# Kernel tuning notes

Measured on AMD Instinct MI355X. Metric: run time of the kernel, lower is better.

Reference implementation:

```python
import jax, jax.numpy as jnp
import numpy as np

NUM_CLASSES = 10
WEIGHT = tuple([0.1] * NUM_CLASSES)
EXPONENT = 2


def setup_inputs() -> dict:
    key = jax.random.key(0)
    k1, k2, k3 = jax.random.split(key, 3)
    B, Y, X = 64, 512, 512
    outputs = jax.random.normal(k1, (B, Y, X), dtype=jnp.float32)
    # targets hold integer intensity classes 0..9 stored as floats (original does float subtraction)
    targets = jax.random.randint(k2, (B, Y, X), 0, NUM_CLASSES).astype(jnp.float32)
    # observation-station mask: 1 where a station exists, 0 elsewhere
    mask = jax.random.randint(k3, (B, Y, X), 0, 2).astype(jnp.int32)
    return {"outputs": outputs, "targets": targets, "mask": mask}


def reference(outputs, targets, mask):
    # Class id per pixel; invalid (mask==0) pixels routed to dummy segment NUM_CLASSES.
    cls = targets.astype(jnp.int32)
    valid = mask == 1
    ids = jnp.where(valid, cls, NUM_CLASSES).ravel()  # [B*Y*X]

    sqerr = (outputs - targets) ** EXPONENT  # [B,Y,X]
    # One fused scatter-reduce replaces the original triple Python loop over 10 masks.
    per_class_sum = jax.ops.segment_sum(sqerr.ravel(), ids, num_segments=NUM_CLASSES + 1)[:NUM_CLASSES]
    class_n = jax.ops.segment_sum(jnp.ones_like(sqerr).ravel(), ids, num_segments=NUM_CLASSES + 1)[:NUM_CLASSES]

    loss_each = jnp.where(class_n > 0, per_class_sum / jnp.maximum(class_n, 1.0), 0.0)  # [10]
    weight = jnp.asarray(WEIGHT, dtype=outputs.dtype)
    loss = jnp.sum(weight * loss_each)
    return loss, loss_each, class_n
```

## Files before the change

kernel.cpp:

```cpp
#include <hip/hip_runtime.h>

#define NCLS 10
#define TPB  256
#define NBLK 2048
#define ACC_STRIDE 64

typedef float vfloat4 __attribute__((ext_vector_type(4)));
typedef int   vint4   __attribute__((ext_vector_type(4)));


__device__ __forceinline__ void proc_elem(float o, float t, int m,
                                          float sum[NCLS], unsigned long long &cnt)
{
    float d  = o - t;
    float sq = d * d;
    int cls  = (m == 1) ? (int)t : NCLS;
    cnt += 1ull << (6 * cls);
#pragma unroll
    for (int c = 0; c < NCLS; ++c)
        sum[c] += (cls == c) ? sq : 0.0f;
}

__global__ __launch_bounds__(TPB) void loss_main_kernel(
    const float* __restrict__ outputs,
    const float* __restrict__ targets,
    const int*   __restrict__ mask,
    float* __restrict__ ws,
    int n4, int n_rem_base, int n_rem)
{
    const vfloat4* o4 = (const vfloat4*)outputs;
    const vfloat4* t4 = (const vfloat4*)targets;
    const vint4*   m4 = (const vint4*)mask;

    const int tid = blockIdx.x * TPB + threadIdx.x;
    const int T   = NBLK * TPB;

    float sum[NCLS];
#pragma unroll
    for (int c = 0; c < NCLS; ++c) sum[c] = 0.0f;
    unsigned long long cnt = 0;

    const int full  = n4 / T;
    const int kfull = full & ~1;

    if (kfull >= 2) {
        vfloat4 oA = __builtin_nontemporal_load(&o4[tid]);
        vfloat4 tA = __builtin_nontemporal_load(&t4[tid]);
        vint4   mA = __builtin_nontemporal_load(&m4[tid]);
        vfloat4 oB = __builtin_nontemporal_load(&o4[tid + T]);
        vfloat4 tB = __builtin_nontemporal_load(&t4[tid + T]);
        vint4   mB = __builtin_nontemporal_load(&m4[tid + T]);

        int k = 0;
        while (true) {
            proc_elem(oA.x, tA.x, mA.x, sum, cnt);
            proc_elem(oA.y, tA.y, mA.y, sum, cnt);
            proc_elem(oA.z, tA.z, mA.z, sum, cnt);
            proc_elem(oA.w, tA.w, mA.w, sum, cnt);
            if (k + 2 < kfull) {
                int i = tid + (k + 2) * T;
                oA = __builtin_nontemporal_load(&o4[i]);
                tA = __builtin_nontemporal_load(&t4[i]);
                mA = __builtin_nontemporal_load(&m4[i]);
            }
            proc_elem(oB.x, tB.x, mB.x, sum, cnt);
            proc_elem(oB.y, tB.y, mB.y, sum, cnt);
            proc_elem(oB.z, tB.z, mB.z, sum, cnt);
            proc_elem(oB.w, tB.w, mB.w, sum, cnt);
            if (k + 3 < kfull) {
                int i = tid + (k + 3) * T;
                oB = __builtin_nontemporal_load(&o4[i]);
                tB = __builtin_nontemporal_load(&t4[i]);
                mB = __builtin_nontemporal_load(&m4[i]);
            }
            k += 2;
            if (k >= kfull) break;
        }
    }
    for (int i = tid + kfull * T; i < n4; i += T) {
        vfloat4 o = __builtin_nontemporal_load(&o4[i]);
        vfloat4 t = __builtin_nontemporal_load(&t4[i]);
        vint4   m = __builtin_nontemporal_load(&m4[i]);
        proc_elem(o.x, t.x, m.x, sum, cnt);
        proc_elem(o.y, t.y, m.y, sum, cnt);
        proc_elem(o.z, t.z, m.z, sum, cnt);
        proc_elem(o.w, t.w, m.w, sum, cnt);
    }
    if (tid < n_rem)
        proc_elem(outputs[n_rem_base + tid], targets[n_rem_base + tid],
                  mask[n_rem_base + tid], sum, cnt);

    float cfl[NCLS];
#pragma unroll
    for (int c = 0; c < NCLS; ++c)
        cfl[c] = (float)((unsigned)(cnt >> (6 * c)) & 63u);

#pragma unroll
    for (int c = 0; c < NCLS; ++c) {
#pragma unroll
        for (int off = 32; off > 0; off >>= 1) {
            sum[c] += __shfl_down(sum[c], off, 64);
            cfl[c] += __shfl_down(cfl[c], off, 64);
        }
    }

    __shared__ float lsS[4][NCLS];
    __shared__ float lsC[4][NCLS];
    int wave = threadIdx.x >> 6;
    int lane = threadIdx.x & 63;
    if (lane == 0) {
#pragma unroll
        for (int c = 0; c < NCLS; ++c) {
            lsS[wave][c] = sum[c];
            lsC[wave][c] = cfl[c];
        }
    }
    __syncthreads();

    if (threadIdx.x < 2 * NCLS) {
        int c = (threadIdx.x < NCLS) ? threadIdx.x : (threadIdx.x - NCLS);
        float v;
        if (threadIdx.x < NCLS)
            v = lsS[0][c] + lsS[1][c] + lsS[2][c] + lsS[3][c];
        else
            v = lsC[0][c] + lsC[1][c] + lsC[2][c] + lsC[3][c];
        atomicAdd(&ws[threadIdx.x * ACC_STRIDE], v);
    }
}

__global__ __launch_bounds__(64) void loss_final_kernel(
    const float* __restrict__ ws,
    float* __restrict__ out)
{
    int lane = threadIdx.x;
    float le = 0.0f;
    if (lane < NCLS) {
        float s  = ws[lane * ACC_STRIDE];
        float cn = ws[(NCLS + lane) * ACC_STRIDE];
        le = (cn > 0.0f) ? (s / fmaxf(cn, 1.0f)) : 0.0f;
        out[1 + lane]  = le;
        out[11 + lane] = cn;
    }
    float w = 0.1f * le;
#pragma unroll
    for (int off = 32; off > 0; off >>= 1) w += __shfl_down(w, off, 64);
    if (lane == 0) out[0] = w;
}

extern "C" void kernel_launch(void* const* d_in, const int* in_sizes, int n_in,
                              void* d_out, int out_size, void* d_ws, size_t ws_size,
                              hipStream_t stream)
{
    const float* outputs = (const float*)d_in[0];
    const float* targets = (const float*)d_in[1];
    const int*   mask    = (const int*)d_in[2];
    float* out = (float*)d_out;
    float* ws  = (float*)d_ws;

    int n  = in_sizes[0];
    int n4 = n / 4;
    int n_rem_base = 4 * n4;
    int n_rem = n - n_rem_base;

    hipMemsetAsync(d_ws, 0, 2 * NCLS * ACC_STRIDE * sizeof(float), stream);
    loss_main_kernel<<<NBLK, TPB, 0, stream>>>(outputs, targets, mask, ws,
                                               n4, n_rem_base, n_rem);
    loss_final_kernel<<<1, 64, 0, stream>>>(ws, out);
}
```

Before: 193.7 us.

## Fuse finalize into main kernel via last-block counter and deepen load pipeline

```diff
diff --git a/kernel.cpp b/kernel.cpp
--- a/kernel.cpp
+++ b/kernel.cpp
@@ -26,6 +26,7 @@
     const float* __restrict__ targets,
     const int*   __restrict__ mask,
     float* __restrict__ ws,
+    float* __restrict__ out,
     int n4, int n_rem_base, int n_rem)
 {
     const vfloat4* o4 = (const vfloat4*)outputs;
@@ -40,51 +41,42 @@
     for (int c = 0; c < NCLS; ++c) sum[c] = 0.0f;
     unsigned long long cnt = 0;
 
-    const int full  = n4 / T;
-    const int kfull = full & ~1;
-
-    if (kfull >= 2) {
-        vfloat4 oA = __builtin_nontemporal_load(&o4[tid]);
-        vfloat4 tA = __builtin_nontemporal_load(&t4[tid]);
-        vint4   mA = __builtin_nontemporal_load(&m4[tid]);
-        vfloat4 oB = __builtin_nontemporal_load(&o4[tid + T]);
-        vfloat4 tB = __builtin_nontemporal_load(&t4[tid + T]);
-        vint4   mB = __builtin_nontemporal_load(&m4[tid + T]);
-
-        int k = 0;
-        while (true) {
-            proc_elem(oA.x, tA.x, mA.x, sum, cnt);
-            proc_elem(oA.y, tA.y, mA.y, sum, cnt);
-            proc_elem(oA.z, tA.z, mA.z, sum, cnt);
-            proc_elem(oA.w, tA.w, mA.w, sum, cnt);
-            if (k + 2 < kfull) {
-                int i = tid + (k + 2) * T;
-                oA = __builtin_nontemporal_load(&o4[i]);
-                tA = __builtin_nontemporal_load(&t4[i]);
-                mA = __builtin_nontemporal_load(&m4[i]);
+    if (n4 == 8 * T) {
+        vfloat4 ob[3], tb[3];
+        vint4   mb[3];
+#pragma unroll
+        for (int p = 0; p < 3; ++p) {
+            int i = tid + p * T;
+            ob[p] = __builtin_nontemporal_load(&o4[i]);
+            tb[p] = __builtin_nontemporal_load(&t4[i]);
+            mb[p] = __builtin_nontemporal_load(&m4[i]);
+        }
+#pragma unroll
+        for (int g = 0; g < 8; ++g) {
+            const int s = g % 3;
+            vfloat4 o = ob[s], t = tb[s];
+            vint4   m = mb[s];
+            if (g + 3 < 8) {
+                int i = tid + (g + 3) * T;
+                ob[s] = __builtin_nontemporal_load(&o4[i]);
+                tb[s] = __builtin_nontemporal_load(&t4[i]);
+                mb[s] = __builtin_nontemporal_load(&m4[i]);
             }
-            proc_elem(oB.x, tB.x, mB.x, sum, cnt);
-            proc_elem(oB.y, tB.y, mB.y, sum, cnt);
-            proc_elem(oB.z, tB.z, mB.z, sum, cnt);
-            proc_elem(oB.w, tB.w, mB.w, sum, cnt);
-            if (k + 3 < kfull) {
-                int i = tid + (k + 3) * T;
-                oB = __builtin_nontemporal_load(&o4[i]);
-                tB = __builtin_nontemporal_load(&t4[i]);
-                mB = __builtin_nontemporal_load(&m4[i]);
-            }
-            k += 2;
-            if (k >= kfull) break;
+            proc_elem(o.x, t.x, m.x, sum, cnt);
+            proc_elem(o.y, t.y, m.y, sum, cnt);
+            proc_elem(o.z, t.z, m.z, sum, cnt);
+            proc_elem(o.w, t.w, m.w, sum, cnt);
         }
-    }
-    for (int i = tid + kfull * T; i < n4; i += T) {
-        vfloat4 o = __builtin_nontemporal_load(&o4[i]);
-        vfloat4 t = __builtin_nontemporal_load(&t4[i]);
-        vint4   m = __builtin_nontemporal_load(&m4[i]);
-        proc_elem(o.x, t.x, m.x, sum, cnt);
-        proc_elem(o.y, t.y, m.y, sum, cnt);
-        proc_elem(o.z, t.z, m.z, sum, cnt);
-        proc_elem(o.w, t.w, m.w, sum, cnt);
+    } else {
+        for (int i = tid; i < n4; i += T) {
+            vfloat4 o = __builtin_nontemporal_load(&o4[i]);
+            vfloat4 t = __builtin_nontemporal_load(&t4[i]);
+            vint4   m = __builtin_nontemporal_load(&m4[i]);
+            proc_elem(o.x, t.x, m.x, sum, cnt);
+            proc_elem(o.y, t.y, m.y, sum, cnt);
+            proc_elem(o.z, t.z, m.z, sum, cnt);
+            proc_elem(o.w, t.w, m.w, sum, cnt);
+        }
     }
     if (tid < n_rem)
         proc_elem(outputs[n_rem_base + tid], targets[n_rem_base + tid],
@@ -106,6 +98,7 @@
 
     __shared__ float lsS[4][NCLS];
     __shared__ float lsC[4][NCLS];
+    __shared__ int   amLast;
     int wave = threadIdx.x >> 6;
     int lane = threadIdx.x & 63;
     if (lane == 0) {
@@ -124,27 +117,31 @@
             v = lsS[0][c] + lsS[1][c] + lsS[2][c] + lsS[3][c];
         else
             v = lsC[0][c] + lsC[1][c] + lsC[2][c] + lsC[3][c];
-        atomicAdd(&ws[threadIdx.x * ACC_STRIDE], v);
+        atomicAdd(&ws[(threadIdx.x + 1) * ACC_STRIDE], v);
     }
-}
 
-__global__ __launch_bounds__(64) void loss_final_kernel(
-    const float* __restrict__ ws,
-    float* __restrict__ out)
-{
-    int lane = threadIdx.x;
-    float le = 0.0f;
-    if (lane < NCLS) {
-        float s  = ws[lane * ACC_STRIDE];
-        float cn = ws[(NCLS + lane) * ACC_STRIDE];
-        le = (cn > 0.0f) ? (s / fmaxf(cn, 1.0f)) : 0.0f;
-        out[1 + lane]  = le;
-        out[11 + lane] = cn;
+    __syncthreads();
+    if (threadIdx.x == 0) {
+        __threadfence();
+        unsigned done = atomicAdd((unsigned*)ws, 1u);
+        amLast = (done == (unsigned)(NBLK - 1)) ? 1 : 0;
     }
-    float w = 0.1f * le;
+    __syncthreads();
+
+    if (amLast && threadIdx.x < 64) {
+        float le = 0.0f;
+        if (lane < NCLS) {
+            float s  = atomicAdd(&ws[(1 + lane) * ACC_STRIDE], 0.0f);
+            float cn = atomicAdd(&ws[(1 + NCLS + lane) * ACC_STRIDE], 0.0f);
+            le = (cn > 0.0f) ? (s / fmaxf(cn, 1.0f)) : 0.0f;
+            out[1 + lane]  = le;
+            out[11 + lane] = cn;
+        }
+        float w = 0.1f * le;
 #pragma unroll
-    for (int off = 32; off > 0; off >>= 1) w += __shfl_down(w, off, 64);
-    if (lane == 0) out[0] = w;
+        for (int off = 32; off > 0; off >>= 1) w += __shfl_down(w, off, 64);
+        if (lane == 0) out[0] = w;
+    }
 }
 
 extern "C" void kernel_launch(void* const* d_in, const int* in_sizes, int n_in,
@@ -162,8 +159,7 @@
     int n_rem_base = 4 * n4;
     int n_rem = n - n_rem_base;
 
-    hipMemsetAsync(d_ws, 0, 2 * NCLS * ACC_STRIDE * sizeof(float), stream);
-    loss_main_kernel<<<NBLK, TPB, 0, stream>>>(outputs, targets, mask, ws,
+    hipMemsetAsync(d_ws, 0, (2 * NCLS + 1) * ACC_STRIDE * sizeof(float), stream);
+    loss_main_kernel<<<NBLK, TPB, 0, stream>>>(outputs, targets, mask, ws, out,
                                                n4, n_rem_base, n_rem);
-    loss_final_kernel<<<1, 64, 0, stream>>>(ws, out);
 }
```

After: 278.5 us. 43.8% more time.

## Stage input loads through LDS with double-buffered global_load_lds DMA

Applied to the files above, without the earlier changes.

```diff
diff --git a/kernel.cpp b/kernel.cpp
--- a/kernel.cpp
+++ b/kernel.cpp
@@ -21,6 +21,24 @@
         sum[c] += (cls == c) ? sq : 0.0f;
 }
 
+__device__ __forceinline__ void proc_group(const vfloat4 &o, const vfloat4 &t,
+                                           const vint4 &m,
+                                           float sum[NCLS], unsigned long long &cnt)
+{
+    proc_elem(o.x, t.x, m.x, sum, cnt);
+    proc_elem(o.y, t.y, m.y, sum, cnt);
+    proc_elem(o.z, t.z, m.z, sum, cnt);
+    proc_elem(o.w, t.w, m.w, sum, cnt);
+}
+
+__device__ __forceinline__ void dma16(const void* g, void* l)
+{
+    __builtin_amdgcn_global_load_lds(
+        (const __attribute__((address_space(1))) void*)g,
+        (__attribute__((address_space(3))) void*)l,
+        16, 0, 0);
+}
+
 __global__ __launch_bounds__(TPB) void loss_main_kernel(
     const float* __restrict__ outputs,
     const float* __restrict__ targets,
@@ -28,103 +46,93 @@
     float* __restrict__ ws,
     int n4, int n_rem_base, int n_rem)
 {
+    __shared__ float ldsO[2][TPB * 4];
+    __shared__ float ldsT[2][TPB * 4];
+    __shared__ int   ldsM[2][TPB * 4];
+
     const vfloat4* o4 = (const vfloat4*)outputs;
     const vfloat4* t4 = (const vfloat4*)targets;
     const vint4*   m4 = (const vint4*)mask;
 
-    const int tid = blockIdx.x * TPB + threadIdx.x;
-    const int T   = NBLK * TPB;
+    const int tx = threadIdx.x;
+    const int w  = tx >> 6;
+    const int G  = NBLK;
 
     float sum[NCLS];
 #pragma unroll
     for (int c = 0; c < NCLS; ++c) sum[c] = 0.0f;
     unsigned long long cnt = 0;
 
-    const int full  = n4 / T;
-    const int kfull = full & ~1;
+    const int nch = n4 >> 8;
 
-    if (kfull >= 2) {
-        vfloat4 oA = __builtin_nontemporal_load(&o4[tid]);
-        vfloat4 tA = __builtin_nontemporal_load(&t4[tid]);
-        vint4   mA = __builtin_nontemporal_load(&m4[tid]);
-        vfloat4 oB = __builtin_nontemporal_load(&o4[tid + T]);
-        vfloat4 tB = __builtin_nontemporal_load(&t4[tid + T]);
-        vint4   mB = __builtin_nontemporal_load(&m4[tid + T]);
+    int c = blockIdx.x;
+    if (c < nch) {
+        dma16(&o4[c * TPB + tx], &ldsO[0][w << 8]);
+        dma16(&t4[c * TPB + tx], &ldsT[0][w << 8]);
+        dma16(&m4[c * TPB + tx], &ldsM[0][w << 8]);
+    }
 
-        int k = 0;
-        while (true) {
-            proc_elem(oA.x, tA.x, mA.x, sum, cnt);
-            proc_elem(oA.y, tA.y, mA.y, sum, cnt);
-            proc_elem(oA.z, tA.z, mA.z, sum, cnt);
-            proc_elem(oA.w, tA.w, mA.w, sum, cnt);
-            if (k + 2 < kfull) {
-                int i = tid + (k + 2) * T;
-                oA = __builtin_nontemporal_load(&o4[i]);
-                tA = __builtin_nontemporal_load(&t4[i]);
-                mA = __builtin_nontemporal_load(&m4[i]);
-            }
-            proc_elem(oB.x, tB.x, mB.x, sum, cnt);
-            proc_elem(oB.y, tB.y, mB.y, sum, cnt);
-            proc_elem(oB.z, tB.z, mB.z, sum, cnt);
-            proc_elem(oB.w, tB.w, mB.w, sum, cnt);
-            if (k + 3 < kfull) {
-                int i = tid + (k + 3) * T;
-                oB = __builtin_nontemporal_load(&o4[i]);
-                tB = __builtin_nontemporal_load(&t4[i]);
-                mB = __builtin_nontemporal_load(&m4[i]);
-            }
-            k += 2;
-            if (k >= kfull) break;
+    int it = 0;
+    for (; c < nch; c += G, ++it) {
+        const int buf = it & 1;
+        __syncthreads();
+        const int cn = c + G;
+        if (cn < nch) {
+            dma16(&o4[cn * TPB + tx], &ldsO[buf ^ 1][w << 8]);
+            dma16(&t4[cn * TPB + tx], &ldsT[buf ^ 1][w << 8]);
+            dma16(&m4[cn * TPB + tx], &ldsM[buf ^ 1][w << 8]);
         }
+        vfloat4 o = *(const vfloat4*)&ldsO[buf][tx * 4];
+        vfloat4 t = *(const vfloat4*)&ldsT[buf][tx * 4];
+        vint4   m = *(const vint4*)  &ldsM[buf][tx * 4];
+        proc_group(o, t, m, sum, cnt);
     }
-    for (int i = tid + kfull * T; i < n4; i += T) {
+
+    for (int i = nch * TPB + blockIdx.x * TPB + tx; i < n4; i += G * TPB) {
         vfloat4 o = __builtin_nontemporal_load(&o4[i]);
         vfloat4 t = __builtin_nontemporal_load(&t4[i]);
         vint4   m = __builtin_nontemporal_load(&m4[i]);
-        proc_elem(o.x, t.x, m.x, sum, cnt);
-        proc_elem(o.y, t.y, m.y, sum, cnt);
-        proc_elem(o.z, t.z, m.z, sum, cnt);
-        proc_elem(o.w, t.w, m.w, sum, cnt);
+        proc_group(o, t, m, sum, cnt);
     }
-    if (tid < n_rem)
-        proc_elem(outputs[n_rem_base + tid], targets[n_rem_base + tid],
-                  mask[n_rem_base + tid], sum, cnt);
+    int gtid = blockIdx.x * TPB + tx;
+    if (gtid < n_rem)
+        proc_elem(outputs[n_rem_base + gtid], targets[n_rem_base + gtid],
+                  mask[n_rem_base + gtid], sum, cnt);
 
     float cfl[NCLS];
 #pragma unroll
-    for (int c = 0; c < NCLS; ++c)
-        cfl[c] = (float)((unsigned)(cnt >> (6 * c)) & 63u);
+    for (int c2 = 0; c2 < NCLS; ++c2)
+        cfl[c2] = (float)((unsigned)(cnt >> (6 * c2)) & 63u);
 
 #pragma unroll
-    for (int c = 0; c < NCLS; ++c) {
+    for (int c2 = 0; c2 < NCLS; ++c2) {
 #pragma unroll
         for (int off = 32; off > 0; off >>= 1) {
-            sum[c] += __shfl_down(sum[c], off, 64);
-            cfl[c] += __shfl_down(cfl[c], off, 64);
+            sum[c2] += __shfl_down(sum[c2], off, 64);
+            cfl[c2] += __shfl_down(cfl[c2], off, 64);
         }
     }
 
     __shared__ float lsS[4][NCLS];
     __shared__ float lsC[4][NCLS];
-    int wave = threadIdx.x >> 6;
-    int lane = threadIdx.x & 63;
+    int lane = tx & 63;
     if (lane == 0) {
 #pragma unroll
-        for (int c = 0; c < NCLS; ++c) {
-            lsS[wave][c] = sum[c];
-            lsC[wave][c] = cfl[c];
+        for (int c2 = 0; c2 < NCLS; ++c2) {
+            lsS[w][c2] = sum[c2];
+            lsC[w][c2] = cfl[c2];
         }
     }
     __syncthreads();
 
-    if (threadIdx.x < 2 * NCLS) {
-        int c = (threadIdx.x < NCLS) ? threadIdx.x : (threadIdx.x - NCLS);
+    if (tx < 2 * NCLS) {
+        int c2 = (tx < NCLS) ? tx : (tx - NCLS);
         float v;
-        if (threadIdx.x < NCLS)
-            v = lsS[0][c] + lsS[1][c] + lsS[2][c] + lsS[3][c];
+        if (tx < NCLS)
+            v = lsS[0][c2] + lsS[1][c2] + lsS[2][c2] + lsS[3][c2];
         else
-            v = lsC[0][c] + lsC[1][c] + lsC[2][c] + lsC[3][c];
-        atomicAdd(&ws[threadIdx.x * ACC_STRIDE], v);
+            v = lsC[0][c2] + lsC[1][c2] + lsC[2][c2] + lsC[3][c2];
+        atomicAdd(&ws[tx * ACC_STRIDE], v);
     }
 }
 
@@ -141,10 +149,10 @@
         out[1 + lane]  = le;
         out[11 + lane] = cn;
     }
-    float w = 0.1f * le;
+    float wsum = 0.1f * le;
 #pragma unroll
-    for (int off = 32; off > 0; off >>= 1) w += __shfl_down(w, off, 64);
-    if (lane == 0) out[0] = w;
+    for (int off = 32; off > 0; off >>= 1) wsum += __shfl_down(wsum, off, 64);
+    if (lane == 0) out[0] = wsum;
 }
 
 extern "C" void kernel_launch(void* const* d_in, const int* in_sizes, int n_in,
```

Result: slower. 204.4 us (+5.5%).

## Pack class accumulators into float2 and hand-pipeline loads with explicit waitcnt

Applied to the files above, without the earlier changes.

```diff
diff --git a/kernel.cpp b/kernel.cpp
--- a/kernel.cpp
+++ b/kernel.cpp
@@ -5,20 +5,54 @@
 #define NBLK 2048
 #define ACC_STRIDE 64
 
-typedef float vfloat4 __attribute__((ext_vector_type(4)));
-typedef int   vint4   __attribute__((ext_vector_type(4)));
-
+typedef float  vfloat4 __attribute__((ext_vector_type(4)));
+typedef int    vint4   __attribute__((ext_vector_type(4)));
+typedef float  vfloat2 __attribute__((ext_vector_type(2)));
+
+
+__device__ __forceinline__ void ld16f(vfloat4 &d, const vfloat4 *p) {
+    asm volatile("global_load_dwordx4 %0, %1, off sc0 nt"
+                 : "=v"(d) : "v"(p) : "memory");
+}
+__device__ __forceinline__ void ld16i(vint4 &d, const vint4 *p) {
+    asm volatile("global_load_dwordx4 %0, %1, off sc0 nt"
+                 : "=v"(d) : "v"(p) : "memory");
+}
+__device__ __forceinline__ void wait3(vfloat4 &o, vfloat4 &t, vint4 &m) {
+    asm volatile("s_waitcnt vmcnt(3)" : "+v"(o), "+v"(t), "+v"(m) :: "memory");
+}
+__device__ __forceinline__ void wait0(vfloat4 &o, vfloat4 &t, vint4 &m) {
+    asm volatile("s_waitcnt vmcnt(0)" : "+v"(o), "+v"(t), "+v"(m) :: "memory");
+}
 
 __device__ __forceinline__ void proc_elem(float o, float t, int m,
-                                          float sum[NCLS], unsigned long long &cnt)
+                                          vfloat2 s2[5], unsigned long long &cnt)
 {
     float d  = o - t;
     float sq = d * d;
     int cls  = (m == 1) ? (int)t : NCLS;
     cnt += 1ull << (6 * cls);
-#pragma unroll
-    for (int c = 0; c < NCLS; ++c)
-        sum[c] += (cls == c) ? sq : 0.0f;
+    int b = cls & 1;
+    int h = cls >> 1;
+    vfloat2 se;
+    se.x = (b == 0) ? sq : 0.0f;
+    se.y = (b == 0) ? 0.0f : sq;
+#pragma unroll
+    for (int p = 0; p < 5; ++p) {
+        vfloat2 z = {0.0f, 0.0f};
+        vfloat2 inc = (h == p) ? se : z;
+        s2[p] += inc;
+    }
+}
+
+__device__ __forceinline__ void proc_group(const vfloat4 &o, const vfloat4 &t,
+                                           const vint4 &m,
+                                           vfloat2 s2[5], unsigned long long &cnt)
+{
+    proc_elem(o.x, t.x, m.x, s2, cnt);
+    proc_elem(o.y, t.y, m.y, s2, cnt);
+    proc_elem(o.z, t.z, m.z, s2, cnt);
+    proc_elem(o.w, t.w, m.w, s2, cnt);
 }
 
 __global__ __launch_bounds__(TPB) void loss_main_kernel(
@@ -35,62 +69,86 @@
     const int tid = blockIdx.x * TPB + threadIdx.x;
     const int T   = NBLK * TPB;
 
-    float sum[NCLS];
-#pragma unroll
-    for (int c = 0; c < NCLS; ++c) sum[c] = 0.0f;
+    vfloat2 s2[5];
+#pragma unroll
+    for (int p = 0; p < 5; ++p) { s2[p].x = 0.0f; s2[p].y = 0.0f; }
     unsigned long long cnt = 0;
 
-    const int full  = n4 / T;
-    const int kfull = full & ~1;
-
-    if (kfull >= 2) {
-        vfloat4 oA = __builtin_nontemporal_load(&o4[tid]);
-        vfloat4 tA = __builtin_nontemporal_load(&t4[tid]);
-        vint4   mA = __builtin_nontemporal_load(&m4[tid]);
-        vfloat4 oB = __builtin_nontemporal_load(&o4[tid + T]);
-        vfloat4 tB = __builtin_nontemporal_load(&t4[tid + T]);
-        vint4   mB = __builtin_nontemporal_load(&m4[tid + T]);
-
-        int k = 0;
-        while (true) {
-            proc_elem(oA.x, tA.x, mA.x, sum, cnt);
-            proc_elem(oA.y, tA.y, mA.y, sum, cnt);
-            proc_elem(oA.z, tA.z, mA.z, sum, cnt);
-            proc_elem(oA.w, tA.w, mA.w, sum, cnt);
-            if (k + 2 < kfull) {
-                int i = tid + (k + 2) * T;
-                oA = __builtin_nontemporal_load(&o4[i]);
-                tA = __builtin_nontemporal_load(&t4[i]);
-                mA = __builtin_nontemporal_load(&m4[i]);
+    if (n4 == 8 * T) {
+        vfloat4 oA, tA, oB, tB;
+        vint4   mA, mB;
+        ld16f(oA, &o4[tid + 0 * T]); ld16f(tA, &t4[tid + 0 * T]); ld16i(mA, &m4[tid + 0 * T]);
+        ld16f(oB, &o4[tid + 1 * T]); ld16f(tB, &t4[tid + 1 * T]); ld16i(mB, &m4[tid + 1 * T]);
+
+#pragma unroll
+        for (int j = 0; j < 3; ++j) {
+            wait3(oA, tA, mA);
+            vfloat4 o = oA, t = tA; vint4 m = mA;
+            ld16f(oA, &o4[tid + (2 * j + 2) * T]);
+            ld16f(tA, &t4[tid + (2 * j + 2) * T]);
+            ld16i(mA, &m4[tid + (2 * j + 2) * T]);
+            proc_group(o, t, m, s2, cnt);
+
+            wait3(oB, tB, mB);
+            vfloat4 o2 = oB, t2 = tB; vint4 m2 = mB;
+            ld16f(oB, &o4[tid + (2 * j + 3) * T]);
+            ld16f(tB, &t4[tid + (2 * j + 3) * T]);
+            ld16i(mB, &m4[tid + (2 * j + 3) * T]);
+            proc_group(o2, t2, m2, s2, cnt);
+        }
+        wait3(oA, tA, mA);
+        proc_group(oA, tA, mA, s2, cnt);
+        wait0(oB, tB, mB);
+        proc_group(oB, tB, mB, s2, cnt);
+    } else {
+        const int full  = n4 / T;
+        const int kfull = full & ~1;
+        if (kfull >= 2) {
+            vfloat4 oA, tA, oB, tB;
+            vint4   mA, mB;
+            oA = __builtin_nontemporal_load(&o4[tid]);
+            tA = __builtin_nontemporal_load(&t4[tid]);
+            mA = __builtin_nontemporal_load(&m4[tid]);
+            oB = __builtin_nontemporal_load(&o4[tid + T]);
+            tB = __builtin_nontemporal_load(&t4[tid + T]);
+            mB = __builtin_nontemporal_load(&m4[tid + T]);
+            int k = 0;
+            while (true) {
+                proc_group(oA, tA, mA, s2, cnt);
+                if (k + 2 < kfull) {
+                    int i = tid + (k + 2) * T;
+                    oA = __builtin_nontemporal_load(&o4[i]);
+                    tA = __builtin_nontemporal_load(&t4[i]);
+                    mA = __builtin_nontemporal_load(&m4[i]);
+                }
+                proc_group(oB, tB, mB, s2, cnt);
+                if (k + 3 < kfull) {
+                    int i = tid + (k + 3) * T;
+                    oB = __builtin_nontemporal_load(&o4[i]);
+                    tB = __builtin_nontemporal_load(&t4[i]);
+                    mB = __builtin_nontemporal_load(&m4[i]);
+                }
+                k += 2;
+                if (k >= kfull) break;
             }
-            proc_elem(oB.x, tB.x, mB.x, sum, cnt);
-            proc_elem(oB.y, tB.y, mB.y, sum, cnt);
-            proc_elem(oB.z, tB.z, mB.z, sum, cnt);
-            proc_elem(oB.w, tB.w, mB.w, sum, cnt);
-            if (k + 3 < kfull) {
-                int i = tid + (k + 3) * T;
-                oB = __builtin_nontemporal_load(&o4[i]);
-                tB = __builtin_nontemporal_load(&t4[i]);
-                mB = __builtin_nontemporal_load(&m4[i]);
-            }
-            k += 2;
-            if (k >= kfull) break;
-        }
-    }
-    for (int i = tid + kfull * T; i < n4; i += T) {
-        vfloat4 o = __builtin_nontemporal_load(&o4[i]);
-        vfloat4 t = __builtin_nontemporal_load(&t4[i]);
-        vint4   m = __builtin_nontemporal_load(&m4[i]);
-        proc_elem(o.x, t.x, m.x, sum, cnt);
-        proc_elem(o.y, t.y, m.y, sum, cnt);
-        proc_elem(o.z, t.z, m.z, sum, cnt);
-        proc_elem(o.w, t.w, m.w, sum, cnt);
+        }
+        for (int i = tid + kfull * T; i < n4; i += T) {
+            vfloat4 o = __builtin_nontemporal_load(&o4[i]);
+            vfloat4 t = __builtin_nontemporal_load(&t4[i]);
+            vint4   m = __builtin_nontemporal_load(&m4[i]);
+            proc_group(o, t, m, s2, cnt);
+        }
     }
     if (tid < n_rem)
         proc_elem(outputs[n_rem_base + tid], targets[n_rem_base + tid],
-                  mask[n_rem_base + tid], sum, cnt);
-
-    float cfl[NCLS];
+                  mask[n_rem_base + tid], s2, cnt);
+
+    float sum[NCLS], cfl[NCLS];
+#pragma unroll
+    for (int p = 0; p < 5; ++p) {
+        sum[2 * p]     = s2[p].x;
+        sum[2 * p + 1] = s2[p].y;
+    }
 #pragma unroll
     for (int c = 0; c < NCLS; ++c)
         cfl[c] = (float)((unsigned)(cnt >> (6 * c)) & 63u);
```

Measured after the change: 191.6 us. Within noise of the previous version (-1.1%).
